# Kernel tuning notes

Hardware: AMD Instinct MI355X
Metric: run time of the kernel (lower is better)

## Reference

```python
import jax, jax.numpy as jnp
import numpy as np

B, C1, C2, H, W = 8, 256, 512, 56, 56

def setup_inputs() -> dict:
    key = jax.random.key(0)
    k1, k2, k3, k4, k5 = jax.random.split(key, 5)
    return {
        "x1": jax.random.normal(k1, (B, C1, H, W), dtype=jnp.float32),
        "x2": jax.random.normal(k2, (B, C2, H, W), dtype=jnp.float32),
        "W_proj": jax.random.normal(k3, (C1, C2), dtype=jnp.float32) * (1.0 / np.sqrt(C2)),
        "b_proj": jax.random.normal(k4, (C1,), dtype=jnp.float32) * 0.01,
        "gamma": jax.random.normal(k5, (1,), dtype=jnp.float32) * 0.1,
    }

def reference(x1, x2, W_proj, b_proj, gamma):
    b, c, h, w = x1.shape
    n = h * w
    # 1x1 conv projection C2 -> C1
    x2p = jnp.einsum('oc,bchw->bohw', W_proj, x2) + b_proj[None, :, None, None]
    query = x1.reshape(b, c, n).transpose(0, 2, 1)   # [B, N, C]
    key_ = x2p.reshape(b, c, n)                      # [B, C, N]
    value = x2p.reshape(b, c, n).transpose(0, 2, 1)  # [B, N, C]
    energy = jnp.einsum('bnc,bcm->bnm', query, key_)  # [B, N, N]
    # inverted-energy softmax: max - energy, then softmax over last dim
    energy_new = jnp.max(energy, axis=-1, keepdims=True) - energy
    attention = jax.nn.softmax(energy_new, axis=-1)
    out = jnp.einsum('bnm,bmc->bnc', attention, value)  # [B, N, C]
    out = out.transpose(0, 2, 1).reshape(b, c, h, w)
    return gamma[0] * out + x1
```

## Files before the change

### kernel.cpp

```cpp
#include <hip/hip_runtime.h>
#include <hip/hip_bf16.h>

#define C1 256
#define C2 512
#define NSP 3136
#define NT 98
#define QT 49

typedef __attribute__((ext_vector_type(8))) short bf16x8;
typedef __attribute__((ext_vector_type(4))) float f32x4;

__device__ __forceinline__ ushort f2b(float f) {
  __hip_bfloat16 h = __float2bfloat16(f);
  return *reinterpret_cast<ushort*>(&h);
}

__device__ __forceinline__ void gload16(const ushort* g, ushort* l) {
  __builtin_amdgcn_global_load_lds(
      (const __attribute__((address_space(1))) void*)g,
      (__attribute__((address_space(3))) void*)l, 16, 0, 0);
}

__global__ __launch_bounds__(256) void k_wtf(const float* __restrict__ W,
                                             ushort* __restrict__ Wf) {
  int ot = blockIdx.x;
  int tid = threadIdx.x;
  int lane = tid & 63, l15 = lane & 15, g = (lane >> 4) & 3;
  int cc0 = (tid >> 6) * 4;
  const float* src = W + (size_t)(ot * 16 + l15) * C2 + g * 8;
#pragma unroll
  for (int k = 0; k < 4; k++) {
    int cc = cc0 + k;
    float4 u0 = *reinterpret_cast<const float4*>(src + cc * 32);
    float4 u1 = *reinterpret_cast<const float4*>(src + cc * 32 + 4);
    bf16x8 v;
    v[0] = (short)f2b(u0.x); v[1] = (short)f2b(u0.y);
    v[2] = (short)f2b(u0.z); v[3] = (short)f2b(u0.w);
    v[4] = (short)f2b(u1.x); v[5] = (short)f2b(u1.y);
    v[6] = (short)f2b(u1.z); v[7] = (short)f2b(u1.w);
    *reinterpret_cast<bf16x8*>(Wf + ((size_t)(ot * 16 + cc)) * 512 + lane * 8) = v;
  }
}

__global__ __launch_bounds__(256) void k_x1t(const float* __restrict__ x1,
                                             ushort* __restrict__ x1t) {
  __shared__ float t[32][33];
  int b = blockIdx.z;
  int n0 = blockIdx.x * 32;
  int c0 = blockIdx.y * 32;
  int tid = threadIdx.x;
  int r = tid >> 3, q = (tid & 7) * 4;
  const float* src = x1 + ((size_t)b * C1 + (c0 + r)) * NSP + n0 + q;
  float4 v = *reinterpret_cast<const float4*>(src);
  t[r][q] = v.x; t[r][q + 1] = v.y; t[r][q + 2] = v.z; t[r][q + 3] = v.w;
  __syncthreads();
  ushort4 o;
  o.x = f2b(t[q + 0][r]); o.y = f2b(t[q + 1][r]);
  o.z = f2b(t[q + 2][r]); o.w = f2b(t[q + 3][r]);
  *reinterpret_cast<ushort4*>(x1t + ((size_t)b * NSP + n0 + r) * C1 + c0 + q) = o;
}

__global__ __launch_bounds__(256) void k_x2f(const float* __restrict__ x2,
                                             ushort* __restrict__ x2f) {
  __shared__ float t[32][33];
  int b = blockIdx.z;
  int n0 = blockIdx.x * 32;
  int cc = blockIdx.y;
  int c0 = cc * 32;
  int tid = threadIdx.x;
  int r = tid >> 3, q = (tid & 7) * 4;
  const float* src = x2 + ((size_t)b * C2 + (c0 + r)) * NSP + n0 + q;
  float4 v = *reinterpret_cast<const float4*>(src);
  t[r][q] = v.x; t[r][q + 1] = v.y; t[r][q + 2] = v.z; t[r][q + 3] = v.w;
  __syncthreads();
  int l15 = tid & 15, g = (tid >> 4) & 3, sub = tid >> 6;
  int ntl = sub & 1, ih = sub >> 1;
  int nl = ntl * 16 + l15;
  int cl = g * 8 + ih * 4;
  ushort4 o;
  o.x = f2b(t[cl + 0][nl]); o.y = f2b(t[cl + 1][nl]);
  o.z = f2b(t[cl + 2][nl]); o.w = f2b(t[cl + 3][nl]);
  int nt16 = (n0 >> 4) + ntl;
  *reinterpret_cast<ushort4*>(
      x2f + (((size_t)b * 196 + nt16) * 16 + cc) * 512 + (size_t)(tid & 63) * 8 + ih * 4) = o;
}

__global__ __launch_bounds__(256) void k_proj(const ushort* __restrict__ Wf,
    const ushort* __restrict__ x2f, const float* __restrict__ bias,
    ushort* __restrict__ Kf, ushort* __restrict__ Vf) {
  __shared__ __align__(16) ushort WL[2][8][512];
  __shared__ __align__(16) ushort XL[2][4][512];
  int bid = blockIdx.x;
  int b = bid & 7;
  int tq = bid >> 3;
  int oh = tq & 1;
  int nt = tq >> 1;
  int tid = threadIdx.x;
  int w = tid >> 6, lane = tid & 63, l15 = lane & 15, g = lane >> 4;
  int wq = w >> 1, wn = w & 1;
  int ot0 = oh * 8;
  int nt0 = nt * 4;

  auto stage = [&](int buf, int cc) {
#pragma unroll
    for (int j = 0; j < 3; j++) {
      int chunk = w * 3 + j;
      if (chunk < 8) {
        gload16(Wf + ((size_t)(ot0 + chunk) * 16 + cc) * 512 + lane * 8,
                &WL[buf][chunk][0]);
      } else {
        gload16(x2f + (((size_t)b * 196 + nt0 + (chunk - 8)) * 16 + cc) * 512 + lane * 8,
                &XL[buf][chunk - 8][0]);
      }
    }
  };

  f32x4 zero = {0.f, 0.f, 0.f, 0.f};
  f32x4 acc[4][2];
#pragma unroll
  for (int a = 0; a < 4; a++)
#pragma unroll
    for (int v = 0; v < 2; v++) acc[a][v] = zero;

  stage(0, 0);
  __syncthreads();

  for (int cc = 0; cc < 16; ++cc) {
    int cur = cc & 1;
    if (cc < 15) stage(cur ^ 1, cc + 1);
    bf16x8 A[4], Bf[2];
#pragma unroll
    for (int a = 0; a < 4; a++)
      A[a] = *reinterpret_cast<const bf16x8*>(&WL[cur][wq * 4 + a][lane * 8]);
#pragma unroll
    for (int v = 0; v < 2; v++)
      Bf[v] = *reinterpret_cast<const bf16x8*>(&XL[cur][wn * 2 + v][lane * 8]);
#pragma unroll
    for (int a = 0; a < 4; a++)
#pragma unroll
      for (int v = 0; v < 2; v++)
        acc[a][v] = __builtin_amdgcn_mfma_f32_16x16x32_bf16(A[a], Bf[v], acc[a][v], 0, 0, 0);
    __syncthreads();
  }

  int obase = oh * 128 + wq * 64;
  float4 bias4[4];
#pragma unroll
  for (int a = 0; a < 4; a++)
    bias4[a] = *reinterpret_cast<const float4*>(&bias[obase + a * 16 + g * 4]);

  int gk = (g & 1) * 4;
#pragma unroll
  for (int a = 0; a < 4; a++) {
    int laneK = (((2 * a + (g >> 1)) & 3) << 4) | l15;
    size_t oK = (size_t)(oh * 4 + wq * 2 + (a >> 1));
#pragma unroll
    for (int v = 0; v < 2; v++) {
      int nK = nt * 4 + wn * 2 + v;
      ushort4 st;
      st.x = f2b(acc[a][v][0] + bias4[a].x);
      st.y = f2b(acc[a][v][1] + bias4[a].y);
      st.z = f2b(acc[a][v][2] + bias4[a].z);
      st.w = f2b(acc[a][v][3] + bias4[a].w);
      *reinterpret_cast<ushort4*>(
          Kf + ((((size_t)b * 196 + nK) * 8 + oK) * 64 + laneK) * 8 + gk) = st;
    }
  }
  int nV = nt * 2 + wn;
#pragma unroll
  for (int v = 0; v < 2; v++) {
    int gv = ((v * 2 + (l15 >> 3)) & 3) << 4;
    int iV = l15 & 7;
#pragma unroll
    for (int a = 0; a < 4; a++) {
      int cs = oh * 8 + wq * 4 + a;
      size_t basev = ((((size_t)b * 98 + nV) * 16 + cs) * 64 + gv) * 8 + iV;
      const float* bp4 = reinterpret_cast<const float*>(&bias4[a]);
#pragma unroll
      for (int r = 0; r < 4; r++)
        Vf[basev + (size_t)(g * 4 + r) * 8] = f2b(acc[a][v][r] + bp4[r]);
    }
  }
}

__global__ __launch_bounds__(256, 2) void k_attn(
    const ushort* __restrict__ x1t, const ushort* __restrict__ Kf,
    const ushort* __restrict__ Vf, const float* __restrict__ x1,
    const float* __restrict__ gamma, float* __restrict__ out) {
  __shared__ __align__(16) ushort Kt[2][8192];
  __shared__ __align__(16) ushort Vt[2][8192];
  __shared__ __align__(16) ushort Plds[4][16][40];
  int bid = blockIdx.x;
  int b = bid & 7;
  int qt = bid >> 3;
  int tid = threadIdx.x;
  int w = tid >> 6;
  int lane = tid & 63;
  int l15 = lane & 15;
  int g = lane >> 4;
  int n0 = qt * 64 + w * 16;
  float gm = gamma[0];

  bf16x8 qf[8];
  const ushort* qb = x1t + ((size_t)b * NSP + n0 + l15) * C1 + g * 8;
#pragma unroll
  for (int cc = 0; cc < 8; cc++)
    qf[cc] = *reinterpret_cast<const bf16x8*>(qb + cc * 32);

  f32x4 zero = {0.f, 0.f, 0.f, 0.f};
  f32x4 O[16];
#pragma unroll
  for (int i = 0; i < 16; i++) O[i] = zero;
  float M[4], L[4];
#pragma unroll
  for (int r = 0; r < 4; r++) { M[r] = -3.0e38f; L[r] = 0.f; }

  const ushort* kg = Kf + (size_t)b * 196 * 8 * 512;
  const ushort* vg = Vf + (size_t)b * 98 * 16 * 512;
  int soff = w * 2048;

  auto stage = [&](int buf, int t) {
    const ushort* ks = kg + (size_t)t * 8192 + soff + lane * 8;
    const ushort* vs = vg + (size_t)t * 8192 + soff + lane * 8;
    ushort* kl = &Kt[buf][soff];
    ushort* vl = &Vt[buf][soff];
#pragma unroll
    for (int j = 0; j < 4; ++j) {
      gload16(ks + j * 512, kl + j * 512);
      gload16(vs + j * 512, vl + j * 512);
    }
  };

  stage(0, 0);
  __syncthreads();

  for (int t = 0; t < NT; ++t) {
    int cur = t & 1;
    if (t + 1 < NT) stage(cur ^ 1, t + 1);

    f32x4 s0a = zero, s0b = zero, s1a = zero, s1b = zero;
    const ushort* kb = &Kt[cur][0];
#pragma unroll
    for (int cc = 0; cc < 8; cc += 2) {
      bf16x8 k00 = *reinterpret_cast<const bf16x8*>(kb + ((size_t)cc * 64 + lane) * 8);
      bf16x8 k10 = *reinterpret_cast<const bf16x8*>(kb + ((size_t)(8 + cc) * 64 + lane) * 8);
      bf16x8 k01 = *reinterpret_cast<const bf16x8*>(kb + ((size_t)(cc + 1) * 64 + lane) * 8);
      bf16x8 k11 = *reinterpret_cast<const bf16x8*>(kb + ((size_t)(9 + cc) * 64 + lane) * 8);
      s0a = __builtin_amdgcn_mfma_f32_16x16x32_bf16(qf[cc], k00, s0a, 0, 0, 0);
      s1a = __builtin_amdgcn_mfma_f32_16x16x32_bf16(qf[cc], k10, s1a, 0, 0, 0);
      s0b = __builtin_amdgcn_mfma_f32_16x16x32_bf16(qf[cc + 1], k01, s0b, 0, 0, 0);
      s1b = __builtin_amdgcn_mfma_f32_16x16x32_bf16(qf[cc + 1], k11, s1b, 0, 0, 0);
    }
    float sc[4];
#pragma unroll
    for (int r = 0; r < 4; r++) {
      float a0 = -(s0a[r] + s0b[r]);
      float a1 = -(s1a[r] + s1b[r]);
      float mx = fmaxf(a0, a1);
      mx = fmaxf(mx, __shfl_xor(mx, 1));
      mx = fmaxf(mx, __shfl_xor(mx, 2));
      mx = fmaxf(mx, __shfl_xor(mx, 4));
      mx = fmaxf(mx, __shfl_xor(mx, 8));
      float nm = fmaxf(M[r], mx);
      sc[r] = __expf(M[r] - nm);
      M[r] = nm;
      float p0 = __expf(a0 - nm);
      float p1 = __expf(a1 - nm);
      Plds[w][g * 4 + r][l15] = f2b(p0);
      Plds[w][g * 4 + r][16 + l15] = f2b(p1);
      float ps = p0 + p1;
      ps += __shfl_xor(ps, 1);
      ps += __shfl_xor(ps, 2);
      ps += __shfl_xor(ps, 4);
      ps += __shfl_xor(ps, 8);
      L[r] = L[r] * sc[r] + ps;
    }
#pragma unroll
    for (int i = 0; i < 16; i++) {
#pragma unroll
      for (int r = 0; r < 4; r++) O[i][r] *= sc[r];
    }
    asm volatile("s_waitcnt lgkmcnt(0)" ::: "memory");
    bf16x8 pf = *reinterpret_cast<const bf16x8*>(&Plds[w][l15][g * 8]);
    const ushort* vb2 = &Vt[cur][0];
#pragma unroll
    for (int cs = 0; cs < 16; ++cs) {
      bf16x8 vf = *reinterpret_cast<const bf16x8*>(vb2 + ((size_t)cs * 64 + lane) * 8);
      O[cs] = __builtin_amdgcn_mfma_f32_16x16x32_bf16(pf, vf, O[cs], 0, 0, 0);
    }
    __syncthreads();
  }

  float rl[4];
#pragma unroll
  for (int r = 0; r < 4; r++) rl[r] = gm / L[r];
  size_t ob = (size_t)b * C1 * NSP + n0 + (size_t)g * 4;
#pragma unroll
  for (int cs = 0; cs < 16; cs++) {
#pragma unroll
    for (int r = 0; r < 4; r++) {
      size_t idx = ob + (size_t)(cs * 16 + l15) * NSP + r;
      out[idx] = O[cs][r] * rl[r] + x1[idx];
    }
  }
}

extern "C" void kernel_launch(void* const* d_in, const int* in_sizes, int n_in,
                              void* d_out, int out_size, void* d_ws, size_t ws_size,
                              hipStream_t stream) {
  const float* x1 = (const float*)d_in[0];
  const float* x2 = (const float*)d_in[1];
  const float* W = (const float*)d_in[2];
  const float* bp = (const float*)d_in[3];
  const float* gamma = (const float*)d_in[4];
  float* out = (float*)d_out;

  char* ws = (char*)d_ws;
  ushort* Wf = (ushort*)(ws + 0);
  ushort* x1t = (ushort*)(ws + 524288);
  ushort* Kf = (ushort*)(ws + 13369344);
  ushort* Vf = (ushort*)(ws + 26214400);
  ushort* x2f = (ushort*)d_out;

  k_wtf<<<dim3(16), dim3(256), 0, stream>>>(W, Wf);
  k_x1t<<<dim3(98, 8, 8), dim3(256), 0, stream>>>(x1, x1t);
  k_x2f<<<dim3(98, 16, 8), dim3(256), 0, stream>>>(x2, x2f);
  k_proj<<<dim3(784), dim3(256), 0, stream>>>(Wf, x2f, bp, Kf, Vf);
  k_attn<<<dim3(392), dim3(256), 0, stream>>>(x1t, Kf, Vf, x1, gamma, out);
}
```

Baseline: 263.4 us.

## Split attention over key range with combine kernel, lazy rescale, MFMA row sums

Measured after the change: 255.6 us. -2.9%, faster.

```diff
diff --git a/kernel.cpp b/kernel.cpp
--- a/kernel.cpp
+++ b/kernel.cpp
@@ -5,7 +5,6 @@
 #define C2 512
 #define NSP 3136
 #define NT 98
-#define QT 49
 
 typedef __attribute__((ext_vector_type(8))) short bf16x8;
 typedef __attribute__((ext_vector_type(4))) float f32x4;
@@ -14,11 +13,18 @@
   __hip_bfloat16 h = __float2bfloat16(f);
   return *reinterpret_cast<ushort*>(&h);
 }
-
+__device__ __forceinline__ float b2f(ushort u) {
+  union { unsigned int i; float f; } v; v.i = ((unsigned int)u) << 16; return v.f;
+}
 __device__ __forceinline__ void gload16(const ushort* g, ushort* l) {
   __builtin_amdgcn_global_load_lds(
       (const __attribute__((address_space(1))) void*)g,
       (__attribute__((address_space(3))) void*)l, 16, 0, 0);
+}
+__device__ __forceinline__ void block_bar() {
+  asm volatile("" ::: "memory");
+  __builtin_amdgcn_s_barrier();
+  asm volatile("" ::: "memory");
 }
 
 __global__ __launch_bounds__(256) void k_wtf(const float* __restrict__ W,
@@ -183,23 +189,27 @@
   }
 }
 
-__global__ __launch_bounds__(256, 2) void k_attn(
+template<int SPLIT>
+__global__ __launch_bounds__(256, 3) void k_attn(
     const ushort* __restrict__ x1t, const ushort* __restrict__ Kf,
     const ushort* __restrict__ Vf, const float* __restrict__ x1,
-    const float* __restrict__ gamma, float* __restrict__ out) {
+    const float* __restrict__ gamma, float* __restrict__ out,
+    ushort* __restrict__ Po, float* __restrict__ Mv, float* __restrict__ Lv) {
   __shared__ __align__(16) ushort Kt[2][8192];
-  __shared__ __align__(16) ushort Vt[2][8192];
-  __shared__ __align__(16) ushort Plds[4][16][40];
+  __shared__ __align__(16) ushort Vt[8192];
+  __shared__ __align__(16) ushort Plds[4][16][36];
   int bid = blockIdx.x;
   int b = bid & 7;
-  int qt = bid >> 3;
+  int qt = SPLIT ? (bid >> 4) : (bid >> 3);
+  int h = SPLIT ? ((bid >> 3) & 1) : 0;
+  int t0 = h * 49;
+  int t1 = SPLIT ? (t0 + 49) : NT;
   int tid = threadIdx.x;
   int w = tid >> 6;
   int lane = tid & 63;
   int l15 = lane & 15;
   int g = lane >> 4;
   int n0 = qt * 64 + w * 16;
-  float gm = gamma[0];
 
   bf16x8 qf[8];
   const ushort* qb = x1t + ((size_t)b * NSP + n0 + l15) * C1 + g * 8;
@@ -211,35 +221,44 @@
   f32x4 O[16];
 #pragma unroll
   for (int i = 0; i < 16; i++) O[i] = zero;
-  float M[4], L[4];
-#pragma unroll
-  for (int r = 0; r < 4; r++) { M[r] = -3.0e38f; L[r] = 0.f; }
+  f32x4 O17 = zero;
+  float M[4];
+#pragma unroll
+  for (int r = 0; r < 4; r++) M[r] = -3.0e38f;
+  bf16x8 onesf;
+#pragma unroll
+  for (int i = 0; i < 8; i++) onesf[i] = (short)0x3F80;
 
   const ushort* kg = Kf + (size_t)b * 196 * 8 * 512;
   const ushort* vg = Vf + (size_t)b * 98 * 16 * 512;
   int soff = w * 2048;
 
-  auto stage = [&](int buf, int t) {
-    const ushort* ks = kg + (size_t)t * 8192 + soff + lane * 8;
-    const ushort* vs = vg + (size_t)t * 8192 + soff + lane * 8;
-    ushort* kl = &Kt[buf][soff];
-    ushort* vl = &Vt[buf][soff];
-#pragma unroll
-    for (int j = 0; j < 4; ++j) {
-      gload16(ks + j * 512, kl + j * 512);
-      gload16(vs + j * 512, vl + j * 512);
-    }
-  };
-
-  stage(0, 0);
-  __syncthreads();
-
-  for (int t = 0; t < NT; ++t) {
-    int cur = t & 1;
-    if (t + 1 < NT) stage(cur ^ 1, t + 1);
+  {
+    const ushort* ks = kg + (size_t)t0 * 8192 + soff + lane * 8;
+#pragma unroll
+    for (int j = 0; j < 4; ++j) gload16(ks + j * 512, &Kt[0][soff] + j * 512);
+  }
+  asm volatile("s_waitcnt vmcnt(0)" ::: "memory");
+  block_bar();
+
+  int cur = 0;
+  for (int t = t0; t < t1; ++t) {
+    {
+      const ushort* vs = vg + (size_t)t * 8192 + soff + lane * 8;
+#pragma unroll
+      for (int j = 0; j < 4; ++j) gload16(vs + j * 512, &Vt[soff] + j * 512);
+    }
+    asm volatile("" ::: "memory");
+    if (t + 1 < t1) {
+      const ushort* ks = kg + (size_t)(t + 1) * 8192 + soff + lane * 8;
+#pragma unroll
+      for (int j = 0; j < 4; ++j) gload16(ks + j * 512, &Kt[cur ^ 1][soff] + j * 512);
+    }
+    asm volatile("" ::: "memory");
 
     f32x4 s0a = zero, s0b = zero, s1a = zero, s1b = zero;
     const ushort* kb = &Kt[cur][0];
+    __builtin_amdgcn_s_setprio(1);
 #pragma unroll
     for (int cc = 0; cc < 8; cc += 2) {
       bf16x8 k00 = *reinterpret_cast<const bf16x8*>(kb + ((size_t)cc * 64 + lane) * 8);
@@ -251,57 +270,129 @@
       s0b = __builtin_amdgcn_mfma_f32_16x16x32_bf16(qf[cc + 1], k01, s0b, 0, 0, 0);
       s1b = __builtin_amdgcn_mfma_f32_16x16x32_bf16(qf[cc + 1], k11, s1b, 0, 0, 0);
     }
-    float sc[4];
+    __builtin_amdgcn_s_setprio(0);
+
+    float a0[4], a1[4], tmax[4];
 #pragma unroll
     for (int r = 0; r < 4; r++) {
-      float a0 = -(s0a[r] + s0b[r]);
-      float a1 = -(s1a[r] + s1b[r]);
-      float mx = fmaxf(a0, a1);
+      a0[r] = -(s0a[r] + s0b[r]);
+      a1[r] = -(s1a[r] + s1b[r]);
+      float mx = fmaxf(a0[r], a1[r]);
       mx = fmaxf(mx, __shfl_xor(mx, 1));
       mx = fmaxf(mx, __shfl_xor(mx, 2));
       mx = fmaxf(mx, __shfl_xor(mx, 4));
       mx = fmaxf(mx, __shfl_xor(mx, 8));
-      float nm = fmaxf(M[r], mx);
-      sc[r] = __expf(M[r] - nm);
-      M[r] = nm;
-      float p0 = __expf(a0 - nm);
-      float p1 = __expf(a1 - nm);
+      tmax[r] = mx;
+    }
+    float d01 = fmaxf(tmax[0] - M[0], tmax[1] - M[1]);
+    float d23 = fmaxf(tmax[2] - M[2], tmax[3] - M[3]);
+    if (__any(fmaxf(d01, d23) > 3.0f)) {
+      float scv[4];
+#pragma unroll
+      for (int r = 0; r < 4; r++) {
+        float nm = fmaxf(M[r], tmax[r]);
+        scv[r] = __expf(M[r] - nm);
+        M[r] = nm;
+      }
+#pragma unroll
+      for (int i = 0; i < 16; i++) {
+#pragma unroll
+        for (int r = 0; r < 4; r++) O[i][r] *= scv[r];
+      }
+#pragma unroll
+      for (int r = 0; r < 4; r++) O17[r] *= scv[r];
+    }
+#pragma unroll
+    for (int r = 0; r < 4; r++) {
+      float p0 = __expf(a0[r] - M[r]);
+      float p1 = __expf(a1[r] - M[r]);
       Plds[w][g * 4 + r][l15] = f2b(p0);
       Plds[w][g * 4 + r][16 + l15] = f2b(p1);
-      float ps = p0 + p1;
-      ps += __shfl_xor(ps, 1);
-      ps += __shfl_xor(ps, 2);
-      ps += __shfl_xor(ps, 4);
-      ps += __shfl_xor(ps, 8);
-      L[r] = L[r] * sc[r] + ps;
-    }
-#pragma unroll
-    for (int i = 0; i < 16; i++) {
-#pragma unroll
-      for (int r = 0; r < 4; r++) O[i][r] *= sc[r];
-    }
-    asm volatile("s_waitcnt lgkmcnt(0)" ::: "memory");
+    }
+
+    if (t + 1 < t1) { asm volatile("s_waitcnt vmcnt(4)" ::: "memory"); }
+    else            { asm volatile("s_waitcnt vmcnt(0)" ::: "memory"); }
+    block_bar();
+
     bf16x8 pf = *reinterpret_cast<const bf16x8*>(&Plds[w][l15][g * 8]);
-    const ushort* vb2 = &Vt[cur][0];
+    __builtin_amdgcn_s_setprio(1);
 #pragma unroll
     for (int cs = 0; cs < 16; ++cs) {
-      bf16x8 vf = *reinterpret_cast<const bf16x8*>(vb2 + ((size_t)cs * 64 + lane) * 8);
+      bf16x8 vf = *reinterpret_cast<const bf16x8*>(&Vt[0] + ((size_t)cs * 64 + lane) * 8);
       O[cs] = __builtin_amdgcn_mfma_f32_16x16x32_bf16(pf, vf, O[cs], 0, 0, 0);
     }
-    __syncthreads();
-  }
-
-  float rl[4];
-#pragma unroll
-  for (int r = 0; r < 4; r++) rl[r] = gm / L[r];
-  size_t ob = (size_t)b * C1 * NSP + n0 + (size_t)g * 4;
-#pragma unroll
-  for (int cs = 0; cs < 16; cs++) {
-#pragma unroll
-    for (int r = 0; r < 4; r++) {
-      size_t idx = ob + (size_t)(cs * 16 + l15) * NSP + r;
-      out[idx] = O[cs][r] * rl[r] + x1[idx];
-    }
+    O17 = __builtin_amdgcn_mfma_f32_16x16x32_bf16(pf, onesf, O17, 0, 0, 0);
+    __builtin_amdgcn_s_setprio(0);
+
+    asm volatile("s_waitcnt vmcnt(0)" ::: "memory");
+    block_bar();
+    cur ^= 1;
+  }
+
+  if (SPLIT) {
+    int pb = bid;
+    int nloc = w * 16 + g * 4;
+#pragma unroll
+    for (int cs = 0; cs < 16; cs++) {
+      int c = cs * 16 + l15;
+      ushort4 st;
+      st.x = f2b(O[cs][0]); st.y = f2b(O[cs][1]);
+      st.z = f2b(O[cs][2]); st.w = f2b(O[cs][3]);
+      *reinterpret_cast<ushort4*>(Po + ((size_t)pb * 256 + c) * 64 + nloc) = st;
+    }
+    if (l15 == 0) {
+#pragma unroll
+      for (int r = 0; r < 4; r++) {
+        Mv[(size_t)pb * 64 + nloc + r] = M[r];
+        Lv[(size_t)pb * 64 + nloc + r] = O17[r];
+      }
+    }
+  } else {
+    float gm = gamma[0];
+    float rl[4];
+#pragma unroll
+    for (int r = 0; r < 4; r++) rl[r] = gm / O17[r];
+    size_t ob = (size_t)b * C1 * NSP + n0 + (size_t)g * 4;
+#pragma unroll
+    for (int cs = 0; cs < 16; cs++) {
+      size_t idx = ob + (size_t)(cs * 16 + l15) * NSP;
+      float4 x4 = *reinterpret_cast<const float4*>(&x1[idx]);
+      float4 o4;
+      o4.x = O[cs][0] * rl[0] + x4.x;
+      o4.y = O[cs][1] * rl[1] + x4.y;
+      o4.z = O[cs][2] * rl[2] + x4.z;
+      o4.w = O[cs][3] * rl[3] + x4.w;
+      *reinterpret_cast<float4*>(&out[idx]) = o4;
+    }
+  }
+}
+
+__global__ __launch_bounds__(256) void k_comb(
+    const ushort* __restrict__ Po, const float* __restrict__ Mv,
+    const float* __restrict__ Lv, const float* __restrict__ x1,
+    const float* __restrict__ gamma, float* __restrict__ out) {
+  int bid = blockIdx.x;
+  int b = bid & 7;
+  int qt = bid >> 3;
+  int tid = threadIdx.x;
+  int n = tid & 63;
+  int c0 = (tid >> 6) * 64;
+  int pb0 = qt * 16 + b;
+  int pb1 = qt * 16 + 8 + b;
+  int n0 = qt * 64;
+  float M0 = Mv[(size_t)pb0 * 64 + n], M1 = Mv[(size_t)pb1 * 64 + n];
+  float L0 = Lv[(size_t)pb0 * 64 + n], L1 = Lv[(size_t)pb1 * 64 + n];
+  float Ms = fmaxf(M0, M1);
+  float w0 = __expf(M0 - Ms), w1 = __expf(M1 - Ms);
+  float rl = gamma[0] / (w0 * L0 + w1 * L1);
+  const ushort* p0 = Po + (size_t)pb0 * 16384 + n;
+  const ushort* p1 = Po + (size_t)pb1 * 16384 + n;
+#pragma unroll 4
+  for (int c = c0; c < c0 + 64; ++c) {
+    float o0 = b2f(p0[(size_t)c * 64]);
+    float o1 = b2f(p1[(size_t)c * 64]);
+    size_t idx = ((size_t)b * C1 + c) * NSP + n0 + n;
+    out[idx] = (w0 * o0 + w1 * o1) * rl + x1[idx];
   }
 }
 
@@ -320,11 +411,22 @@
   ushort* x1t = (ushort*)(ws + 524288);
   ushort* Kf = (ushort*)(ws + 13369344);
   ushort* Vf = (ushort*)(ws + 26214400);
+  ushort* Po = (ushort*)(ws + 39059456);
+  float* Mv = (float*)(ws + 64749568);
+  float* Lv = (float*)(ws + 64950272);
   ushort* x2f = (ushort*)d_out;
 
   k_wtf<<<dim3(16), dim3(256), 0, stream>>>(W, Wf);
   k_x1t<<<dim3(98, 8, 8), dim3(256), 0, stream>>>(x1, x1t);
   k_x2f<<<dim3(98, 16, 8), dim3(256), 0, stream>>>(x2, x2f);
   k_proj<<<dim3(784), dim3(256), 0, stream>>>(Wf, x2f, bp, Kf, Vf);
-  k_attn<<<dim3(392), dim3(256), 0, stream>>>(x1t, Kf, Vf, x1, gamma, out);
-}
+
+  if (ws_size >= 65150976ULL) {
+    k_attn<1><<<dim3(784), dim3(256), 0, stream>>>(x1t, Kf, Vf, x1, gamma, out,
+                                                   Po, Mv, Lv);
+    k_comb<<<dim3(392), dim3(256), 0, stream>>>(Po, Mv, Lv, x1, gamma, out);
+  } else {
+    k_attn<0><<<dim3(392), dim3(256), 0, stream>>>(x1t, Kf, Vf, x1, gamma, out,
+                                                   Po, Mv, Lv);
+  }
+}
```
